# Kernel tuning notes

Measured on AMD Instinct MI355X. Metric: run time of the kernel, lower is better.

The kernel has to match this reference:

```python
import jax, jax.numpy as jnp
import numpy as np
import itertools

# ---- static configuration (matches init_kwargs) ----
LS = [0, 1, 2, 3]            # spherical harmonic degrees, parity (-1)^l
MUL = 128                    # channel multiplicity of hklm / output
N_EDGES = 16384
DIMS = [2 * l + 1 for l in LS]
Y_DIM = sum(DIMS)                        # 16
H_DIM = sum(d * MUL for d in DIMS)       # 2048
Y_OFF = np.cumsum([0] + DIMS).tolist()
H_OFF = np.cumsum([0] + [d * MUL for d in DIMS]).tolist()

# ---- real-basis O(3) Clebsch-Gordan coefficients (numpy, setup-time) ----
def _su2_generators(l):
    m = np.arange(-l, l + 1)
    Lz = np.diag(m).astype(np.complex128)
    vals = np.sqrt(l * (l + 1) - m[:-1] * (m[:-1] + 1))
    Lp = np.zeros((2 * l + 1, 2 * l + 1), np.complex128)
    Lp[np.arange(1, 2 * l + 1), np.arange(2 * l)] = vals
    Lm = Lp.T.copy()
    return (Lp + Lm) / 2.0, (Lp - Lm) / 2.0j, Lz

def _c2r(l):
    # unitary change of basis: complex SH -> real SH
    d = 2 * l + 1
    U = np.zeros((d, d), np.complex128)
    U[l, l] = 1.0
    s2 = 1.0 / np.sqrt(2.0)
    for m in range(1, l + 1):
        U[l + m, l + m] = (-1) ** m * s2
        U[l + m, l - m] = s2
        U[l - m, l + m] = -1j * (-1) ** m * s2
        U[l - m, l - m] = 1j * s2
    return U

def _real_generators(l):
    U = _c2r(l)
    return [np.real(-1j * (U @ L @ U.conj().T)) for L in _su2_generators(l)]

def _cg(l1, l2, l3):
    # invariant tensor = null space of the summed infinitesimal rotation action
    G1, G2, G3 = _real_generators(l1), _real_generators(l2), _real_generators(l3)
    d1, d2, d3 = 2 * l1 + 1, 2 * l2 + 1, 2 * l3 + 1
    I1, I2, I3 = np.eye(d1), np.eye(d2), np.eye(d3)
    rows = []
    for k in range(3):
        rows.append(np.kron(np.kron(G1[k], I2), I3)
                    + np.kron(np.kron(I1, G2[k]), I3)
                    + np.kron(np.kron(I1, I2), G3[k]))
    K = np.concatenate(rows, axis=0)
    _, s, Vt = np.linalg.svd(K)
    c = Vt[-1].reshape(d1, d2, d3)
    c = c / np.linalg.norm(c)
    c = c * np.sign(c.reshape(-1)[np.argmax(np.abs(c))])  # deterministic sign
    return c

PATHS = []
_CG_LIST = []
for (i1, l1), (i2, l2), (i3, l3) in itertools.product(enumerate(LS), enumerate(LS), enumerate(LS)):
    # triangle inequality + O3 parity selection rule ((-1)^l parities)
    if abs(l1 - l2) <= l3 <= l1 + l2 and (l1 + l2 + l3) % 2 == 0:
        PATHS.append((i1, i2, i3))
        _CG_LIST.append(_cg(l1, l2, l3))
N_PATHS = len(PATHS)                    # 23
W_DIM = N_PATHS * MUL                   # 2944
CG_OFF = np.cumsum([0] + [c.size for c in _CG_LIST]).tolist()
CGC_NP = np.concatenate([c.reshape(-1) for c in _CG_LIST]).astype(np.float32)


def setup_inputs() -> dict:
    key = jax.random.key(0)
    k1, k2, k3 = jax.random.split(key, 3)
    return {
        "Ylm": jax.random.normal(k1, (N_EDGES, Y_DIM), jnp.float32),
        "hklm": jax.random.normal(k2, (N_EDGES, H_DIM), jnp.float32),
        "weight": jax.random.normal(k3, (N_EDGES, W_DIM), jnp.float32),
        "CGC": jnp.asarray(CGC_NP),   # registered buffer in the torch module
    }


def reference(Ylm, hklm, weight, CGC):
    # segmented tensor product 'abcu,a,bu,cu' with per-path weight fused in:
    # out[n, c, u] += sum_{a,b} CG_p[a,b,c] * w_p[n,u] * Y[n,a] * h[n,b,u]
    N = Ylm.shape[0]
    out = jnp.zeros((N, H_DIM), Ylm.dtype)
    for p, (i1, i2, i3) in enumerate(PATHS):
        d1, d2, d3 = DIMS[i1], DIMS[i2], DIMS[i3]
        cg = CGC[CG_OFF[p]:CG_OFF[p + 1]].reshape(d1, d2, d3)
        y = Ylm[:, Y_OFF[i1]:Y_OFF[i1] + d1]
        h = hklm[:, H_OFF[i2]:H_OFF[i2] + d2 * MUL].reshape(N, d2, MUL)
        w = weight[:, p * MUL:(p + 1) * MUL]
        z = jnp.einsum('abc,na,nbu->ncu', cg, y, h) * w[:, None, :]
        out = out.at[:, H_OFF[i3]:H_OFF[i3] + d3 * MUL].add(z.reshape(N, d3 * MUL))
    return out
```

## Files before the change

kernel.cpp:

```cpp
#include <hip/hip_runtime.h>


#define BS 256
#define EPB 4
#define TPE 64
#define YD 16
#define HD 2048
#define WD 2944
#define NROW 99

typedef float f2 __attribute__((ext_vector_type(2)));
typedef float f4 __attribute__((ext_vector_type(4)));

#define FOR_PATHS(X) \
  X(0, 0,0,0,    0,  0) \
  X(1, 0,1,1,    1,  1) \
  X(2, 0,2,2,   10,  4) \
  X(3, 0,3,3,   35,  9) \
  X(4, 1,0,1,   84, 16) \
  X(5, 1,1,0,   93, 19) \
  X(6, 1,1,2,  102, 20) \
  X(7, 1,2,1,  147, 25) \
  X(8, 1,2,3,  192, 28) \
  X(9, 1,3,2,  297, 35) \
  X(10,2,0,2,  402, 40) \
  X(11,2,1,1,  427, 45) \
  X(12,2,1,3,  472, 48) \
  X(13,2,2,0,  577, 55) \
  X(14,2,2,2,  602, 56) \
  X(15,2,3,1,  727, 61) \
  X(16,2,3,3,  832, 64) \
  X(17,3,0,3, 1077, 71) \
  X(18,3,1,2, 1126, 78) \
  X(19,3,2,1, 1231, 83) \
  X(20,3,2,3, 1336, 86) \
  X(21,3,3,0, 1581, 93) \
  X(22,3,3,2, 1630, 94)

__host__ __device__ constexpr int coff(int l) {
  return l == 0 ? 0 : (l == 1 ? 1 : (l == 2 ? 4 : 9));
}

__global__ __launch_bounds__(BS, 4) void etp_kernel(
    const float* __restrict__ Y, const float* __restrict__ H,
    const float* __restrict__ W, const float* __restrict__ CG,
    float* __restrict__ O) {
  const int g = threadIdx.x >> 6;
  const int l = threadIdx.x & 63;
  const size_t n = (size_t)blockIdx.x * EPB + g;

  __shared__ __align__(16) float Bsm[EPB][NROW * 8];
  __shared__ float ysm[EPB][YD];

  { const int t = threadIdx.x;
    if (t < EPB * YD) {
      const int e = t >> 4, c = t & 15;
      ysm[e][c] = Y[(size_t)(blockIdx.x * EPB + e) * YD + c];
    } }
  __syncthreads();

#define BUILD(P, L1, L2, L3, CGO, RO) { \
    constexpr int d1 = 2*(L1)+1, d2 = 2*(L2)+1, d3 = 2*(L3)+1; \
    if (l < d2 * d3) { \
      const int m3 = l / d2, m2 = l - m3 * d2; \
      float s = 0.f; \
      _Pragma("unroll") \
      for (int a = 0; a < d1; ++a) \
        s += CG[(CGO) + (a * d2 + m2) * d3 + m3] * ysm[g][coff(L1) + a]; \
      Bsm[g][((RO) + m3) * 8 + m2] = s; \
    } }
  FOR_PATHS(BUILD)
#undef BUILD
  __syncthreads();

  const f2* __restrict__ Hp = (const f2*)(H + n * HD);
  const f2* __restrict__ Wp = (const f2*)(W + n * WD);
  f2* __restrict__ Op = (f2*)(O + n * HD);

  f2 acc[YD];
#pragma unroll
  for (int c = 0; c < YD; ++c) acc[c] = (f2)0.f;

#define DOP(P, L2, L3, RO) { \
    constexpr int d2 = 2*(L2)+1, d3 = 2*(L3)+1; \
    const f2 wv = Wp[(P) * TPE + l]; \
    _Pragma("unroll") \
    for (int m3 = 0; m3 < d3; ++m3) { \
      const f4* row = (const f4*)&Bsm[g][((RO) + m3) * 8]; \
      float br[8]; \
      *(f4*)&br[0] = row[0]; \
      if (d2 > 4) *(f4*)&br[4] = row[1]; \
      f2 s = (f2)0.f; \
      _Pragma("unroll") \
      for (int m2 = 0; m2 < d2; ++m2) s += br[m2] * hh[m2]; \
      acc[coff(L3) + m3] += s * wv; \
    } }

  {
    f2 hh[1];
    hh[0] = Hp[(coff(0) + 0) * TPE + l];
    DOP(0, 0, 0, 0)  DOP(4, 0, 1, 16)  DOP(10, 0, 2, 40)  DOP(17, 0, 3, 71)
  }
  {
    f2 hh[3];
#pragma unroll
    for (int m = 0; m < 3; ++m) hh[m] = Hp[(coff(1) + m) * TPE + l];
    DOP(1, 1, 1, 1)  DOP(5, 1, 0, 19)  DOP(6, 1, 2, 20)
    DOP(11, 1, 1, 45)  DOP(12, 1, 3, 48)  DOP(18, 1, 2, 78)
  }
  {
    f2 hh[5];
#pragma unroll
    for (int m = 0; m < 5; ++m) hh[m] = Hp[(coff(2) + m) * TPE + l];
    DOP(2, 2, 2, 4)  DOP(7, 2, 1, 25)  DOP(8, 2, 3, 28)
    DOP(13, 2, 0, 55)  DOP(14, 2, 2, 56)  DOP(19, 2, 1, 83)  DOP(20, 2, 3, 86)
  }
  {
    f2 hh[7];
#pragma unroll
    for (int m = 0; m < 7; ++m) hh[m] = Hp[(coff(3) + m) * TPE + l];
    DOP(3, 3, 3, 9)  DOP(9, 3, 2, 35)  DOP(15, 3, 1, 61)
    DOP(16, 3, 3, 64)  DOP(21, 3, 0, 93)  DOP(22, 3, 2, 94)
  }
#undef DOP

#pragma unroll
  for (int c = 0; c < YD; ++c)
    __builtin_nontemporal_store(acc[c], &Op[c * TPE + l]);
}

extern "C" void kernel_launch(void* const* d_in, const int* in_sizes, int n_in,
                              void* d_out, int out_size, void* d_ws, size_t ws_size,
                              hipStream_t stream) {
  const float* Y  = (const float*)d_in[0];
  const float* H  = (const float*)d_in[1];
  const float* W  = (const float*)d_in[2];
  const float* CG = (const float*)d_in[3];
  float* O = (float*)d_out;

  const int n_edges = in_sizes[0] / YD;
  etp_kernel<<<n_edges / EPB, BS, 0, stream>>>(Y, H, W, CG, O);
}
```

Baseline: 109.3 us.

## Split per-edge CG-Y matrix build into separate kernel via global workspace

```diff
diff --git a/kernel.cpp b/kernel.cpp
--- a/kernel.cpp
+++ b/kernel.cpp
@@ -7,58 +7,157 @@
 #define YD 16
 #define HD 2048
 #define WD 2944
-#define NROW 99
+#define BF4 160
+#define BFLOAT (BF4 * 4)
+#define WS_NEED ((size_t)16384 * BFLOAT * 4)
 
 typedef float f2 __attribute__((ext_vector_type(2)));
 typedef float f4 __attribute__((ext_vector_type(4)));
 
 #define FOR_PATHS(X) \
-  X(0, 0,0,0,    0,  0) \
-  X(1, 0,1,1,    1,  1) \
-  X(2, 0,2,2,   10,  4) \
-  X(3, 0,3,3,   35,  9) \
-  X(4, 1,0,1,   84, 16) \
-  X(5, 1,1,0,   93, 19) \
-  X(6, 1,1,2,  102, 20) \
-  X(7, 1,2,1,  147, 25) \
-  X(8, 1,2,3,  192, 28) \
-  X(9, 1,3,2,  297, 35) \
-  X(10,2,0,2,  402, 40) \
-  X(11,2,1,1,  427, 45) \
-  X(12,2,1,3,  472, 48) \
-  X(13,2,2,0,  577, 55) \
-  X(14,2,2,2,  602, 56) \
-  X(15,2,3,1,  727, 61) \
-  X(16,2,3,3,  832, 64) \
-  X(17,3,0,3, 1077, 71) \
-  X(18,3,1,2, 1126, 78) \
-  X(19,3,2,1, 1231, 83) \
-  X(20,3,2,3, 1336, 86) \
-  X(21,3,3,0, 1581, 93) \
-  X(22,3,3,2, 1630, 94)
+  X(0, 0,0,0,    0,   0) \
+  X(1, 0,1,1,    1,   1) \
+  X(2, 0,2,2,   10,   4) \
+  X(3, 0,3,3,   35,  14) \
+  X(4, 1,0,1,   84,  28) \
+  X(5, 1,1,0,   93,  31) \
+  X(6, 1,1,2,  102,  32) \
+  X(7, 1,2,1,  147,  37) \
+  X(8, 1,2,3,  192,  43) \
+  X(9, 1,3,2,  297,  57) \
+  X(10,2,0,2,  402,  67) \
+  X(11,2,1,1,  427,  72) \
+  X(12,2,1,3,  472,  75) \
+  X(13,2,2,0,  577,  82) \
+  X(14,2,2,2,  602,  84) \
+  X(15,2,3,1,  727,  94) \
+  X(16,2,3,3,  832, 100) \
+  X(17,3,0,3, 1077, 114) \
+  X(18,3,1,2, 1126, 121) \
+  X(19,3,2,1, 1231, 126) \
+  X(20,3,2,3, 1336, 132) \
+  X(21,3,3,0, 1581, 146) \
+  X(22,3,3,2, 1630, 148)
 
 __host__ __device__ constexpr int coff(int l) {
   return l == 0 ? 0 : (l == 1 ? 1 : (l == 2 ? 4 : 9));
 }
 
+__global__ __launch_bounds__(BS) void build_kernel(
+    const float* __restrict__ Y, const float* __restrict__ CG,
+    float* __restrict__ Bws) {
+  const int wid = threadIdx.x >> 6;
+  const int l = threadIdx.x & 63;
+  const size_t n = (size_t)blockIdx.x * EPB + wid;
+
+  float yv = Y[n * YD + (l & 15)];
+  float yy[YD];
+#pragma unroll
+  for (int c = 0; c < YD; ++c) yy[c] = __shfl(yv, c, 64);
+
+  float* B = Bws + n * BFLOAT;
+#define BLD(P, L1, L2, L3, CGO, RO4) { \
+    constexpr int d1 = 2*(L1)+1, d2 = 2*(L2)+1, d3 = 2*(L3)+1; \
+    constexpr int rs = (d2 > 4) ? 2 : 1; \
+    if (l < d2 * d3) { \
+      const int m3 = l / d2, m2 = l - m3 * d2; \
+      float s = 0.f; \
+      _Pragma("unroll") \
+      for (int a = 0; a < d1; ++a) \
+        s += CG[(CGO) + (a * d2 + m2) * d3 + m3] * yy[coff(L1) + a]; \
+      B[((RO4) + m3 * rs) * 4 + m2] = s; \
+    } }
+  FOR_PATHS(BLD)
+#undef BLD
+}
+
 __global__ __launch_bounds__(BS, 4) void etp_kernel(
+    const float* __restrict__ H, const float* __restrict__ W,
+    const float* __restrict__ Bws, float* __restrict__ O) {
+  const int g = threadIdx.x >> 6;
+  const int l = threadIdx.x & 63;
+  const size_t n = (size_t)blockIdx.x * EPB + g;
+
+  const f4* __restrict__ Bp = (const f4*)(Bws + n * BFLOAT);
+  const f2* __restrict__ Hp = (const f2*)(H + n * HD);
+  const f2* __restrict__ Wp = (const f2*)(W + n * WD);
+  f2* __restrict__ Op = (f2*)(O + n * HD);
+
+  f2 acc[YD];
+#pragma unroll
+  for (int c = 0; c < YD; ++c) acc[c] = (f2)0.f;
+
+#define DOP(P, L2, L3, RO4) { \
+    constexpr int d2 = 2*(L2)+1, d3 = 2*(L3)+1; \
+    constexpr int rs = (d2 > 4) ? 2 : 1; \
+    const f2 wv = Wp[(P) * TPE + l]; \
+    _Pragma("unroll") \
+    for (int m3 = 0; m3 < d3; ++m3) { \
+      float br[8]; \
+      *(f4*)&br[0] = Bp[(RO4) + m3 * rs]; \
+      if (d2 > 4) *(f4*)&br[4] = Bp[(RO4) + m3 * rs + 1]; \
+      f2 s = (f2)0.f; \
+      _Pragma("unroll") \
+      for (int m2 = 0; m2 < d2; ++m2) s += br[m2] * hh[m2]; \
+      acc[coff(L3) + m3] += s * wv; \
+    } }
+
+  {
+    f2 hh[1];
+    hh[0] = Hp[(coff(0) + 0) * TPE + l];
+    DOP(0, 0, 0, 0)  DOP(4, 0, 1, 28)  DOP(10, 0, 2, 67)  DOP(17, 0, 3, 114)
+  }
+  {
+    f2 hh[3];
+#pragma unroll
+    for (int m = 0; m < 3; ++m) hh[m] = Hp[(coff(1) + m) * TPE + l];
+    DOP(1, 1, 1, 1)  DOP(5, 1, 0, 31)  DOP(6, 1, 2, 32)
+    DOP(11, 1, 1, 72)  DOP(12, 1, 3, 75)  DOP(18, 1, 2, 121)
+  }
+  {
+    f2 hh[5];
+#pragma unroll
+    for (int m = 0; m < 5; ++m) hh[m] = Hp[(coff(2) + m) * TPE + l];
+    DOP(2, 2, 2, 4)  DOP(7, 2, 1, 37)  DOP(8, 2, 3, 43)
+    DOP(13, 2, 0, 82)  DOP(14, 2, 2, 84)  DOP(19, 2, 1, 126)  DOP(20, 2, 3, 132)
+  }
+  {
+    f2 hh[7];
+#pragma unroll
+    for (int m = 0; m < 7; ++m) hh[m] = Hp[(coff(3) + m) * TPE + l];
+    DOP(3, 3, 3, 14)  DOP(9, 3, 2, 57)  DOP(15, 3, 1, 94)
+    DOP(16, 3, 3, 100)  DOP(21, 3, 0, 146)  DOP(22, 3, 2, 148)
+  }
+#undef DOP
+
+#pragma unroll
+  for (int c = 0; c < YD; ++c)
+    __builtin_nontemporal_store(acc[c], &Op[c * TPE + l]);
+}
+
+#define NROW 99
+__global__ __launch_bounds__(BS, 4) void etp_fallback(
     const float* __restrict__ Y, const float* __restrict__ H,
     const float* __restrict__ W, const float* __restrict__ CG,
     float* __restrict__ O) {
   const int g = threadIdx.x >> 6;
   const int l = threadIdx.x & 63;
   const size_t n = (size_t)blockIdx.x * EPB + g;
-
   __shared__ __align__(16) float Bsm[EPB][NROW * 8];
   __shared__ float ysm[EPB][YD];
-
   { const int t = threadIdx.x;
     if (t < EPB * YD) {
       const int e = t >> 4, c = t & 15;
       ysm[e][c] = Y[(size_t)(blockIdx.x * EPB + e) * YD + c];
     } }
   __syncthreads();
-
+#define FOR_PATHS_OLD(X) \
+  X(0,0,0,0,0,0) X(1,0,1,1,1,1) X(2,0,2,2,10,4) X(3,0,3,3,35,9) \
+  X(4,1,0,1,84,16) X(5,1,1,0,93,19) X(6,1,1,2,102,20) X(7,1,2,1,147,25) \
+  X(8,1,2,3,192,28) X(9,1,3,2,297,35) X(10,2,0,2,402,40) X(11,2,1,1,427,45) \
+  X(12,2,1,3,472,48) X(13,2,2,0,577,55) X(14,2,2,2,602,56) X(15,2,3,1,727,61) \
+  X(16,2,3,3,832,64) X(17,3,0,3,1077,71) X(18,3,1,2,1126,78) X(19,3,2,1,1231,83) \
+  X(20,3,2,3,1336,86) X(21,3,3,0,1581,93) X(22,3,3,2,1630,94)
 #define BUILD(P, L1, L2, L3, CGO, RO) { \
     constexpr int d1 = 2*(L1)+1, d2 = 2*(L2)+1, d3 = 2*(L3)+1; \
     if (l < d2 * d3) { \
@@ -69,18 +168,15 @@
         s += CG[(CGO) + (a * d2 + m2) * d3 + m3] * ysm[g][coff(L1) + a]; \
       Bsm[g][((RO) + m3) * 8 + m2] = s; \
     } }
-  FOR_PATHS(BUILD)
+  FOR_PATHS_OLD(BUILD)
 #undef BUILD
   __syncthreads();
-
   const f2* __restrict__ Hp = (const f2*)(H + n * HD);
   const f2* __restrict__ Wp = (const f2*)(W + n * WD);
   f2* __restrict__ Op = (f2*)(O + n * HD);
-
   f2 acc[YD];
 #pragma unroll
   for (int c = 0; c < YD; ++c) acc[c] = (f2)0.f;
-
 #define DOP(P, L2, L3, RO) { \
     constexpr int d2 = 2*(L2)+1, d3 = 2*(L3)+1; \
     const f2 wv = Wp[(P) * TPE + l]; \
@@ -95,35 +191,21 @@
       for (int m2 = 0; m2 < d2; ++m2) s += br[m2] * hh[m2]; \
       acc[coff(L3) + m3] += s * wv; \
     } }
-
-  {
-    f2 hh[1];
-    hh[0] = Hp[(coff(0) + 0) * TPE + l];
-    DOP(0, 0, 0, 0)  DOP(4, 0, 1, 16)  DOP(10, 0, 2, 40)  DOP(17, 0, 3, 71)
-  }
-  {
-    f2 hh[3];
-#pragma unroll
-    for (int m = 0; m < 3; ++m) hh[m] = Hp[(coff(1) + m) * TPE + l];
-    DOP(1, 1, 1, 1)  DOP(5, 1, 0, 19)  DOP(6, 1, 2, 20)
-    DOP(11, 1, 1, 45)  DOP(12, 1, 3, 48)  DOP(18, 1, 2, 78)
-  }
-  {
-    f2 hh[5];
-#pragma unroll
-    for (int m = 0; m < 5; ++m) hh[m] = Hp[(coff(2) + m) * TPE + l];
-    DOP(2, 2, 2, 4)  DOP(7, 2, 1, 25)  DOP(8, 2, 3, 28)
-    DOP(13, 2, 0, 55)  DOP(14, 2, 2, 56)  DOP(19, 2, 1, 83)  DOP(20, 2, 3, 86)
-  }
-  {
-    f2 hh[7];
-#pragma unroll
-    for (int m = 0; m < 7; ++m) hh[m] = Hp[(coff(3) + m) * TPE + l];
-    DOP(3, 3, 3, 9)  DOP(9, 3, 2, 35)  DOP(15, 3, 1, 61)
-    DOP(16, 3, 3, 64)  DOP(21, 3, 0, 93)  DOP(22, 3, 2, 94)
-  }
+  { f2 hh[1]; hh[0] = Hp[0 * TPE + l];
+    DOP(0,0,0,0) DOP(4,0,1,16) DOP(10,0,2,40) DOP(17,0,3,71) }
+  { f2 hh[3];
+#pragma unroll
+    for (int m = 0; m < 3; ++m) hh[m] = Hp[(1 + m) * TPE + l];
+    DOP(1,1,1,1) DOP(5,1,0,19) DOP(6,1,2,20) DOP(11,1,1,45) DOP(12,1,3,48) DOP(18,1,2,78) }
+  { f2 hh[5];
+#pragma unroll
+    for (int m = 0; m < 5; ++m) hh[m] = Hp[(4 + m) * TPE + l];
+    DOP(2,2,2,4) DOP(7,2,1,25) DOP(8,2,3,28) DOP(13,2,0,55) DOP(14,2,2,56) DOP(19,2,1,83) DOP(20,2,3,86) }
+  { f2 hh[7];
+#pragma unroll
+    for (int m = 0; m < 7; ++m) hh[m] = Hp[(9 + m) * TPE + l];
+    DOP(3,3,3,9) DOP(9,3,2,35) DOP(15,3,1,61) DOP(16,3,3,64) DOP(21,3,0,93) DOP(22,3,2,94) }
 #undef DOP
-
 #pragma unroll
   for (int c = 0; c < YD; ++c)
     __builtin_nontemporal_store(acc[c], &Op[c * TPE + l]);
@@ -139,5 +221,13 @@
   float* O = (float*)d_out;
 
   const int n_edges = in_sizes[0] / YD;
-  etp_kernel<<<n_edges / EPB, BS, 0, stream>>>(Y, H, W, CG, O);
-}
+  const int blocks = n_edges / EPB;
+
+  if (ws_size >= WS_NEED) {
+    float* Bws = (float*)d_ws;
+    build_kernel<<<blocks, BS, 0, stream>>>(Y, CG, Bws);
+    etp_kernel<<<blocks, BS, 0, stream>>>(H, W, Bws, O);
+  } else {
+    etp_fallback<<<blocks, BS, 0, stream>>>(Y, H, W, CG, O);
+  }
+}
```

Result: slower. 196.2 us (+79.5%).
